# Kernel optimization log

Hardware: AMD Instinct MI355X
Metric: run time of the kernel (lower is better)

The kernel has to match this reference:

```python
import jax, jax.numpy as jnp
import numpy as np

S = 8192      # sequence length
D = 768       # bert_out_dim
NA = 256      # num aspects
NO = 256      # num opinions
MAXW = 40     # max span width (width_embedding has 40 entries)
NCAT = 13
NPOL = 3


def setup_inputs() -> dict:
    key = jax.random.key(0)
    ks = jax.random.split(key, 9)
    word_rep = jax.random.normal(ks[0], (S, D), jnp.float32)
    a_head = jax.random.randint(ks[1], (NA,), 0, S - MAXW)
    a_w = jax.random.randint(ks[2], (NA,), 1, MAXW + 1)
    aspects = jnp.stack([a_head, a_head + a_w], axis=-1)  # [NA,2] (head,tail), head<tail
    o_head = jax.random.randint(ks[3], (NO,), 0, S - MAXW)
    o_w = jax.random.randint(ks[4], (NO,), 1, MAXW + 1)
    opinions = jnp.stack([o_head, o_head + o_w], axis=-1)  # [NO,2]
    sc = 0.02
    return {
        'word_rep': word_rep,
        'aspects': aspects,
        'opinions': opinions,
        'W_valid': jax.random.normal(ks[5], (2 * D, 2), jnp.float32) * sc,
        'b_valid': jnp.zeros((2,), jnp.float32),
        'W_cat': jax.random.normal(ks[6], (2 * D, NCAT), jnp.float32) * sc,
        'b_cat': jnp.zeros((NCAT,), jnp.float32),
        'W_pol': jax.random.normal(ks[7], (2 * D, NPOL), jnp.float32) * sc,
        'b_pol': jnp.zeros((NPOL,), jnp.float32),
    }


def _span_maxpool(word_rep, spans):
    # variable-width span max-pool over tokens, vectorized with a gather + mask
    heads, tails = spans[:, 0], spans[:, 1]          # [n]
    pos = heads[:, None] + jnp.arange(MAXW)[None, :]  # [n, MAXW]
    valid = pos < tails[:, None]                      # [n, MAXW]
    g = word_rep[jnp.clip(pos, 0, word_rep.shape[0] - 1)]  # [n, MAXW, D]
    neg = jnp.finfo(word_rep.dtype).min
    return jnp.max(jnp.where(valid[:, :, None], g, neg), axis=1)  # [n, D]


def reference(word_rep, aspects, opinions, W_valid, b_valid, W_cat, b_cat, W_pol, b_pol):
    asp_rep = _span_maxpool(word_rep, aspects)   # [NA, D]
    opi_rep = _span_maxpool(word_rep, opinions)  # [NO, D]
    na, no = asp_rep.shape[0], opi_rep.shape[0]
    # all aspect x opinion pairs (itertools.product order): asp varies slowest
    pair_reps = jnp.concatenate([
        jnp.repeat(asp_rep, no, axis=0),          # [NA*NO, D]
        jnp.tile(opi_rep, (na, 1)),               # [NA*NO, D]
    ], axis=-1)                                    # [NA*NO, 2D]
    asp_ids = jnp.repeat(jnp.arange(na), no)
    opi_ids = jnp.tile(jnp.arange(no), na)

    valid_out = pair_reps @ W_valid + b_valid      # [P, 2]
    cate_out = pair_reps @ W_cat + b_cat           # [P, NCAT]
    polar_out = pair_reps @ W_pol + b_pol          # [P, NPOL]

    valid_mask = valid_out[:, 0] > valid_out[:, 1]  # [P] bool
    # jit-safe masking instead of data-dependent boolean select
    m = valid_mask[:, None]
    return (jnp.where(m, pair_reps, 0.0),
            jnp.where(valid_mask, asp_ids, -1),
            jnp.where(valid_mask, opi_ids, -1),
            jnp.where(m, cate_out, 0.0),
            jnp.where(m, polar_out, 0.0),
            valid_mask)
```

## Files before the change

### kernel.cpp

```cpp
#include <hip/hip_runtime.h>
#include <math.h>

#define S 8192
#define D 768
#define NA 256
#define NO 256
#define MAXW 40
#define NCAT 13
#define NPOL 3
#define NPROJ (2 + NCAT + NPOL)

#define OFF1 ((size_t)NA * NO * 2 * D)
#define OFF2 (OFF1 + (size_t)NA * NO)
#define OFF3 (OFF2 + (size_t)NA * NO)
#define OFF4 (OFF3 + (size_t)NA * NO * NCAT)
#define OFF5 (OFF4 + (size_t)NA * NO * NPOL)

typedef float vfloat4 __attribute__((ext_vector_type(4)));

__global__ __launch_bounds__(256) void span_pool_proj(
    const float* __restrict__ word_rep,
    const int*   __restrict__ aspects,
    const int*   __restrict__ opinions,
    const float* __restrict__ W_valid,
    const float* __restrict__ W_cat,
    const float* __restrict__ W_pol,
    float*  __restrict__ rep_out,
    double* __restrict__ proj_out)
{
    __shared__ float rep[D];
    const int b = blockIdx.x;
    const int t = threadIdx.x;

    const int* spans = (b < NA) ? aspects : opinions;
    const int  s     = (b < NA) ? b : (b - NA);
    const int  woff  = (b < NA) ? 0 : D;

    const int head  = spans[2 * s];
    const int tail  = spans[2 * s + 1];
    const int width = tail - head;

    if (t < 192) {
        const vfloat4* base = (const vfloat4*)(word_rep + (size_t)head * D) + t;
        vfloat4 m = base[0];
        for (int r = 1; r < width; ++r) {
            vfloat4 v = base[(size_t)r * (D / 4)];
            m.x = fmaxf(m.x, v.x); m.y = fmaxf(m.y, v.y);
            m.z = fmaxf(m.z, v.z); m.w = fmaxf(m.w, v.w);
        }
        ((vfloat4*)rep)[t] = m;
        ((vfloat4*)(rep_out + (size_t)b * D))[t] = m;
    }
    __syncthreads();

    if (t < NPROJ) {
        const float* W; int ncol, col;
        if (t < 2)             { W = W_valid; ncol = 2;    col = t; }
        else if (t < 2 + NCAT) { W = W_cat;   ncol = NCAT; col = t - 2; }
        else                   { W = W_pol;   ncol = NPOL; col = t - 2 - NCAT; }
        double a0 = 0.0, a1 = 0.0;
        for (int d = 0; d < D; d += 2) {
            a0 += (double)rep[d]     * (double)W[(size_t)(woff + d)     * ncol + col];
            a1 += (double)rep[d + 1] * (double)W[(size_t)(woff + d + 1) * ncol + col];
        }
        proj_out[(size_t)b * NPROJ + t] = a0 + a1;
    }
}

__global__ __launch_bounds__(256) void pair_small(
    const double* __restrict__ proj,
    const float*  __restrict__ b_valid,
    const float*  __restrict__ b_cat,
    const float*  __restrict__ b_pol,
    float*    __restrict__ out,
    unsigned* __restrict__ maskbuf)
{
    const int i = blockIdx.x;
    const int j = threadIdx.x;
    const int p = (i << 8) | j;

    const double* pa = proj + (size_t)i * NPROJ;
    const double* po = proj + (size_t)(NA + j) * NPROJ;

    const double v0 = pa[0] + po[0] + (double)b_valid[0];
    const double v1 = pa[1] + po[1] + (double)b_valid[1];
    const int mask = (v0 > v1) ? 1 : 0;

    maskbuf[p] = (unsigned)mask;
    out[OFF1 + p] = mask ? (float)i : -1.0f;
    out[OFF2 + p] = mask ? (float)j : -1.0f;
    out[OFF5 + p] = mask ? 1.0f : 0.0f;
#pragma unroll
    for (int c = 0; c < NCAT; ++c) {
        float v = mask ? (float)(pa[2 + c] + po[2 + c] + (double)b_cat[c]) : 0.0f;
        out[OFF3 + (size_t)p * NCAT + c] = v;
    }
#pragma unroll
    for (int c = 0; c < NPOL; ++c) {
        float v = mask ? (float)(pa[2 + NCAT + c] + po[2 + NCAT + c] + (double)b_pol[c]) : 0.0f;
        out[OFF4 + (size_t)p * NPOL + c] = v;
    }
}

__global__ __launch_bounds__(384) void pair_stream(
    const vfloat4*  __restrict__ rep4,
    const unsigned* __restrict__ maskbuf,
    vfloat4*        __restrict__ out4)
{
    const int p = blockIdx.x;
    const int t = threadIdx.x;
    const int i = p >> 8;
    const int j = p & 255;

    vfloat4 val = (vfloat4)0.f;
    if (maskbuf[p]) {
        val = (t < 192) ? rep4[(size_t)i * 192 + t]
                        : rep4[(size_t)(NA + j) * 192 + (t - 192)];
    }
    __builtin_nontemporal_store(val, &out4[(size_t)p * 384 + t]);
}

extern "C" void kernel_launch(void* const* d_in, const int* in_sizes, int n_in,
                              void* d_out, int out_size, void* d_ws, size_t ws_size,
                              hipStream_t stream)
{
    const float* word_rep = (const float*)d_in[0];
    const int*   aspects  = (const int*)  d_in[1];
    const int*   opinions = (const int*)  d_in[2];
    const float* W_valid  = (const float*)d_in[3];
    const float* b_valid  = (const float*)d_in[4];
    const float* W_cat    = (const float*)d_in[5];
    const float* b_cat    = (const float*)d_in[6];
    const float* W_pol    = (const float*)d_in[7];
    const float* b_pol    = (const float*)d_in[8];
    float* out = (float*)d_out;

    float*    rep  = (float*)d_ws;
    double*   proj = (double*)((char*)d_ws + (size_t)(NA + NO) * D * sizeof(float));
    unsigned* mask = (unsigned*)((char*)proj + (size_t)(NA + NO) * NPROJ * sizeof(double));

    span_pool_proj<<<NA + NO, 256, 0, stream>>>(
        word_rep, aspects, opinions, W_valid, W_cat, W_pol, rep, proj);

    pair_small<<<NA, NO, 0, stream>>>(proj, b_valid, b_cat, b_pol, out, mask);

    pair_stream<<<NA * NO, 384, 0, stream>>>((const vfloat4*)rep, mask, (vfloat4*)out);
}
```

Measured before the change: 474.1 us.

## Fuse pair mask/small-output and streaming kernels; split projection across warps

```diff
diff --git a/kernel.cpp b/kernel.cpp
--- a/kernel.cpp
+++ b/kernel.cpp
@@ -16,6 +16,8 @@
 #define OFF4 (OFF3 + (size_t)NA * NO * NCAT)
 #define OFF5 (OFF4 + (size_t)NA * NO * NPOL)
 
+#define NEGF (-3.402823466e+38f)
+
 typedef float vfloat4 __attribute__((ext_vector_type(4)));
 
 __global__ __launch_bounds__(256) void span_pool_proj(
@@ -28,7 +30,8 @@
     float*  __restrict__ rep_out,
     double* __restrict__ proj_out)
 {
-    __shared__ float rep[D];
+    __shared__ float  rep[D];
+    __shared__ double part[4][NPROJ];
     const int b = blockIdx.x;
     const int t = threadIdx.x;
 
@@ -43,81 +46,104 @@
     if (t < 192) {
         const vfloat4* base = (const vfloat4*)(word_rep + (size_t)head * D) + t;
         vfloat4 m = base[0];
-        for (int r = 1; r < width; ++r) {
+#pragma unroll
+        for (int r = 1; r < MAXW; ++r) {
             vfloat4 v = base[(size_t)r * (D / 4)];
-            m.x = fmaxf(m.x, v.x); m.y = fmaxf(m.y, v.y);
-            m.z = fmaxf(m.z, v.z); m.w = fmaxf(m.w, v.w);
+            const bool ok = r < width;
+            m.x = fmaxf(m.x, ok ? v.x : NEGF);
+            m.y = fmaxf(m.y, ok ? v.y : NEGF);
+            m.z = fmaxf(m.z, ok ? v.z : NEGF);
+            m.w = fmaxf(m.w, ok ? v.w : NEGF);
         }
         ((vfloat4*)rep)[t] = m;
         ((vfloat4*)(rep_out + (size_t)b * D))[t] = m;
     }
     __syncthreads();
 
-    if (t < NPROJ) {
+    const int w    = t >> 6;
+    const int lane = t & 63;
+    if (lane < NPROJ) {
         const float* W; int ncol, col;
-        if (t < 2)             { W = W_valid; ncol = 2;    col = t; }
-        else if (t < 2 + NCAT) { W = W_cat;   ncol = NCAT; col = t - 2; }
-        else                   { W = W_pol;   ncol = NPOL; col = t - 2 - NCAT; }
+        if (lane < 2)           { W = W_valid; ncol = 2;    col = lane; }
+        else if (lane < 2+NCAT) { W = W_cat;   ncol = NCAT; col = lane - 2; }
+        else                    { W = W_pol;   ncol = NPOL; col = lane - 2 - NCAT; }
+        const int d0 = w * (D / 4);
         double a0 = 0.0, a1 = 0.0;
-        for (int d = 0; d < D; d += 2) {
+#pragma unroll 8
+        for (int d = d0; d < d0 + (D / 4); d += 2) {
             a0 += (double)rep[d]     * (double)W[(size_t)(woff + d)     * ncol + col];
             a1 += (double)rep[d + 1] * (double)W[(size_t)(woff + d + 1) * ncol + col];
         }
-        proj_out[(size_t)b * NPROJ + t] = a0 + a1;
+        part[w][lane] = a0 + a1;
     }
+    __syncthreads();
+    if (t < NPROJ)
+        proj_out[(size_t)b * NPROJ + t] =
+            (part[0][t] + part[1][t]) + (part[2][t] + part[3][t]);
 }
 
-__global__ __launch_bounds__(256) void pair_small(
-    const double* __restrict__ proj,
-    const float*  __restrict__ b_valid,
-    const float*  __restrict__ b_cat,
-    const float*  __restrict__ b_pol,
-    float*    __restrict__ out,
-    unsigned* __restrict__ maskbuf)
+#define JPB 64
+
+__global__ __launch_bounds__(384) void pair_out(
+    const vfloat4* __restrict__ rep4,
+    const double*  __restrict__ proj,
+    const float*   __restrict__ b_valid,
+    const float*   __restrict__ b_cat,
+    const float*   __restrict__ b_pol,
+    float*         __restrict__ out)
 {
-    const int i = blockIdx.x;
-    const int j = threadIdx.x;
-    const int p = (i << 8) | j;
+    const int blk = blockIdx.x;
+    const int i   = blk >> 2;
+    const int j0  = (blk & 3) * JPB;
+    const int t   = threadIdx.x;
 
-    const double* pa = proj + (size_t)i * NPROJ;
-    const double* po = proj + (size_t)(NA + j) * NPROJ;
+    const double pa0 = proj[(size_t)i * NPROJ + 0];
+    const double pa1 = proj[(size_t)i * NPROJ + 1];
+    const double bv0 = (double)b_valid[0];
+    const double bv1 = (double)b_valid[1];
 
-    const double v0 = pa[0] + po[0] + (double)b_valid[0];
-    const double v1 = pa[1] + po[1] + (double)b_valid[1];
-    const int mask = (v0 > v1) ? 1 : 0;
+    vfloat4 av = (vfloat4)0.f;
+    if (t < 192) av = rep4[(size_t)i * 192 + t];
 
-    maskbuf[p] = (unsigned)mask;
-    out[OFF1 + p] = mask ? (float)i : -1.0f;
-    out[OFF2 + p] = mask ? (float)j : -1.0f;
-    out[OFF5 + p] = mask ? 1.0f : 0.0f;
-#pragma unroll
-    for (int c = 0; c < NCAT; ++c) {
-        float v = mask ? (float)(pa[2 + c] + po[2 + c] + (double)b_cat[c]) : 0.0f;
-        out[OFF3 + (size_t)p * NCAT + c] = v;
+    const int c = t - 192;
+    double pac = 0.0; float bias = 0.0f;
+    if (c >= 0 && c < 16) {
+        pac  = proj[(size_t)i * NPROJ + 2 + c];
+        bias = (c < NCAT) ? b_cat[c] : b_pol[c - NCAT];
     }
-#pragma unroll
-    for (int c = 0; c < NPOL; ++c) {
-        float v = mask ? (float)(pa[2 + NCAT + c] + po[2 + NCAT + c] + (double)b_pol[c]) : 0.0f;
-        out[OFF4 + (size_t)p * NPOL + c] = v;
+
+    const double* po  = proj + (size_t)(NA + j0) * NPROJ;
+    vfloat4*      dst = (vfloat4*)out + (size_t)((i << 8) | j0) * 384 + t;
+
+    for (int jj = 0; jj < JPB; ++jj) {
+        const int j = j0 + jj;
+        const int p = (i << 8) | j;
+
+        const double v0 = pa0 + po[0] + bv0;
+        const double v1 = pa1 + po[1] + bv1;
+        const bool mask = v0 > v1;
+
+        vfloat4 val = (vfloat4)0.f;
+        if (mask)
+            val = (t < 192) ? av
+                            : rep4[(size_t)(NA + j) * 192 + (t - 192)];
+        __builtin_nontemporal_store(val, dst);
+
+        if (c >= 0 && c < 16) {
+            float v = mask ? (float)(pac + po[2 + c] + (double)bias) : 0.0f;
+            if (c < NCAT) out[OFF3 + (size_t)p * NCAT + c] = v;
+            else          out[OFF4 + (size_t)p * NPOL + (c - NCAT)] = v;
+        } else if (c == 16) {
+            out[OFF1 + p] = mask ? (float)i : -1.0f;
+        } else if (c == 17) {
+            out[OFF2 + p] = mask ? (float)j : -1.0f;
+        } else if (c == 18) {
+            out[OFF5 + p] = mask ? 1.0f : 0.0f;
+        }
+
+        po  += NPROJ;
+        dst += 384;
     }
-}
-
-__global__ __launch_bounds__(384) void pair_stream(
-    const vfloat4*  __restrict__ rep4,
-    const unsigned* __restrict__ maskbuf,
-    vfloat4*        __restrict__ out4)
-{
-    const int p = blockIdx.x;
-    const int t = threadIdx.x;
-    const int i = p >> 8;
-    const int j = p & 255;
-
-    vfloat4 val = (vfloat4)0.f;
-    if (maskbuf[p]) {
-        val = (t < 192) ? rep4[(size_t)i * 192 + t]
-                        : rep4[(size_t)(NA + j) * 192 + (t - 192)];
-    }
-    __builtin_nontemporal_store(val, &out4[(size_t)p * 384 + t]);
 }
 
 extern "C" void kernel_launch(void* const* d_in, const int* in_sizes, int n_in,
@@ -135,14 +161,12 @@
     const float* b_pol    = (const float*)d_in[8];
     float* out = (float*)d_out;
 
-    float*    rep  = (float*)d_ws;
-    double*   proj = (double*)((char*)d_ws + (size_t)(NA + NO) * D * sizeof(float));
-    unsigned* mask = (unsigned*)((char*)proj + (size_t)(NA + NO) * NPROJ * sizeof(double));
+    float*  rep  = (float*)d_ws;
+    double* proj = (double*)((char*)d_ws + (size_t)(NA + NO) * D * sizeof(float));
 
     span_pool_proj<<<NA + NO, 256, 0, stream>>>(
         word_rep, aspects, opinions, W_valid, W_cat, W_pol, rep, proj);
 
-    pair_small<<<NA, NO, 0, stream>>>(proj, b_valid, b_cat, b_pol, out, mask);
-
-    pair_stream<<<NA * NO, 384, 0, stream>>>((const vfloat4*)rep, mask, (vfloat4*)out);
+    pair_out<<<NA * 4, 384, 0, stream>>>(
+        (const vfloat4*)rep, proj, b_valid, b_cat, b_pol, out);
 }
```

Result: faster. 463.5 us (-2.2%).
